# Kernel tuning notes

Measured on AMD Instinct MI355X. Metric: run time of the kernel, lower is better.

Reference implementation:

```python
import jax, jax.numpy as jnp
import numpy as np

NUM_POINTS = 100000
BATCH = 4096
K = 10


def setup_inputs() -> dict:
    key = jax.random.key(0)
    k1, k2, k3, k4, k5 = jax.random.split(key, 5)
    rays_o = jax.random.normal(k1, (BATCH, 3), dtype=jnp.float32)
    rays_d = jax.random.normal(k2, (BATCH, 3), dtype=jnp.float32)
    xyz = jax.random.normal(k3, (NUM_POINTS, 3), dtype=jnp.float32) * 0.1
    features_dc = jax.random.normal(k4, (NUM_POINTS, 1, 3), dtype=jnp.float32)
    opacity = jax.random.normal(k5, (NUM_POINTS, 1), dtype=jnp.float32)
    return {"rays_o": rays_o, "rays_d": rays_d, "xyz": xyz,
            "features_dc": features_dc, "opacity": opacity}


def reference(rays_o, rays_d, xyz, features_dc, opacity):
    # colors = sigmoid(features[:,0,:]) ; features[:,0,:] == features_dc[:,0,:]
    colors = jax.nn.sigmoid(features_dc[:, 0, :])          # [N,3]
    op = jax.nn.sigmoid(opacity[:, 0])                      # [N]
    ray_centers = rays_o + rays_d * 3.0                     # [B,3]
    # Euclidean cdist via ||a||^2 + ||b||^2 - 2 a.b (matmul form, like torch.cdist p=2)
    sq = (jnp.sum(ray_centers * ray_centers, axis=1)[:, None]
          + jnp.sum(xyz * xyz, axis=1)[None, :]
          - 2.0 * ray_centers @ xyz.T)                      # [B,N]
    distances = jnp.sqrt(jnp.maximum(sq, 0.0))
    # top-K smallest distances per ray
    _, idx = jax.lax.top_k(-distances, K)                   # [B,K]
    d_sel = jnp.take_along_axis(distances, idx, axis=1)     # [B,K]
    w = jnp.exp(-d_sel * 0.1) * op[idx]                     # [B,K]
    w = w / (jnp.sum(w, axis=1, keepdims=True) + 1e-8)
    rgb = jnp.einsum('bk,bkc->bc', w, colors[idx])          # [B,3]
    return rgb
```

## Files before the change

kernel.cpp:

```cpp
#include <hip/hip_runtime.h>
#include <math.h>

#define NPTS   100000
#define NRAYS  4096
#define KTOP   10
#define KMER   12
#define CAP    128
#define LCAP   12

#define PPAIR  4
#define SBLK   49
#define RCS    64
#define RPBS   (NRAYS / RCS)

#define TPAIR  4
#define NPART  64
#define TRAYS  8
#define TGRP   16

typedef float v2f __attribute__((ext_vector_type(2)));

static_assert(SBLK * 2048 >= NPTS, "scan covers all points");
static_assert(TGRP * 2048 <= NPTS, "theta sample within real points");

__device__ __forceinline__ float4 make_center(const float* __restrict__ ro,
                                              const float* __restrict__ rd,
                                              int ray, float w) {
    float ox = ro[3 * ray + 0], oy = ro[3 * ray + 1], oz = ro[3 * ray + 2];
    float dx = rd[3 * ray + 0], dy = rd[3 * ray + 1], dz = rd[3 * ray + 2];
    float cx, cy, cz;
    {
#pragma clang fp contract(off)
        cx = ox + dx * 3.0f;
        cy = oy + dy * 3.0f;
        cz = oz + dz * 3.0f;
    }
    return make_float4(cx, cy, cz, w);
}

__device__ __forceinline__ float sigm(float x) { return 1.0f / (1.0f + expf(-x)); }

__device__ __forceinline__ float rfl(float x) {
    return __int_as_float(__builtin_amdgcn_readfirstlane(__float_as_int(x)));
}

__device__ __forceinline__ v2f score2(v2f px, v2f py, v2f pz, v2f pw,
                                      v2f rx, v2f ry, v2f rz) {
    v2f t = __builtin_elementwise_fma(pz, rz, pw);
    t = __builtin_elementwise_fma(py, ry, t);
    return __builtin_elementwise_fma(px, rx, t);
}

__device__ __forceinline__ unsigned long long mkkey(float sc, int id, bool v) {
    unsigned u = __float_as_uint(sc);
    u = (u & 0x80000000u) ? ~u : (u | 0x80000000u);
    unsigned long long k = ((unsigned long long)u << 32) | (unsigned)(~id);
    return v ? k : 0ull;
}

__global__ __launch_bounds__(256, 2) void theta_kernel(const float* __restrict__ xyz,
                                                       const float* __restrict__ ro,
                                                       const float* __restrict__ rd,
                                                       float4* __restrict__ c4,
                                                       int* __restrict__ cnt) {
    __shared__ float4 rsh[TRAYS];
    __shared__ float  Msh[4][TRAYS][64];
    const int tid = threadIdx.x, wave = tid >> 6, lane = tid & 63;
    const int rbase = blockIdx.x * TRAYS;

    if (tid < TRAYS) rsh[tid] = make_center(ro, rd, rbase + tid, 0.0f);
    __syncthreads();

    float4 rr[TRAYS];
#pragma unroll
    for (int r = 0; r < TRAYS; ++r) rr[r] = rsh[r];

    v2f M[TRAYS];
#pragma unroll
    for (int r = 0; r < TRAYS; ++r) M[r] = (v2f){-INFINITY, -INFINITY};

#pragma unroll 1
    for (int g = 0; g < TGRP; g += 2) {
        v2f px[2][TPAIR], py[2][TPAIR], pz[2][TPAIR], pw[2][TPAIR];
#pragma unroll
        for (int h = 0; h < 2; ++h) {
            const int id0 = (g + h) * 2048 + wave * 512 + lane;
#pragma unroll
            for (int u = 0; u < TPAIR; ++u) {
                int ia = id0 + (2 * u) * 64, ib = id0 + (2 * u + 1) * 64;
                float xa = xyz[3 * ia + 0], ya = xyz[3 * ia + 1], za = xyz[3 * ia + 2];
                float xb = xyz[3 * ib + 0], yb = xyz[3 * ib + 1], zb = xyz[3 * ib + 2];
                px[h][u] = (v2f){xa, xb}; py[h][u] = (v2f){ya, yb}; pz[h][u] = (v2f){za, zb};
                pw[h][u] = (v2f){-0.5f * fmaf(xa, xa, fmaf(ya, ya, za * za)),
                                 -0.5f * fmaf(xb, xb, fmaf(yb, yb, zb * zb))};
            }
        }
#pragma unroll
        for (int r = 0; r < TRAYS; ++r) {
            const v2f rx = (v2f){rr[r].x, rr[r].x};
            const v2f ry = (v2f){rr[r].y, rr[r].y};
            const v2f rz = (v2f){rr[r].z, rr[r].z};
            v2f m = M[r];
#pragma unroll
            for (int h = 0; h < 2; ++h) {
#pragma unroll
                for (int u = 0; u < TPAIR; ++u) {
                    v2f t = __builtin_elementwise_fma(pz[h][u], rz, pw[h][u]);
                    t = __builtin_elementwise_fma(py[h][u], ry, t);
                    t = __builtin_elementwise_fma(px[h][u], rx, t);
                    m = __builtin_elementwise_max(m, t);
                }
            }
            M[r] = m;
        }
    }

#pragma unroll
    for (int r = 0; r < TRAYS; ++r)
        Msh[wave][r][lane] = fmaxf(M[r].x, M[r].y);
    __syncthreads();

    if (tid < TRAYS) {
        float vs[KTOP];
#pragma unroll
        for (int j = 0; j < KTOP; ++j) vs[j] = -INFINITY;
#pragma unroll 1
        for (int p = 0; p < NPART; ++p) {
            float v = fmaxf(fmaxf(Msh[0][tid][p], Msh[1][tid][p]),
                            fmaxf(Msh[2][tid][p], Msh[3][tid][p]));
#pragma unroll
            for (int t = KTOP - 1; t >= 1; --t) {
                bool up = v > vs[t - 1], here = v > vs[t];
                vs[t] = up ? vs[t - 1] : (here ? v : vs[t]);
            }
            vs[0] = fmaxf(vs[0], v);
        }
        float4 c = rsh[tid];
        c.w = vs[KTOP - 1];
        c4[rbase + tid] = c;
        cnt[rbase + tid] = 0;
    }
}

__global__ __launch_bounds__(256, 6) void scan_kernel(const float* __restrict__ xyz,
                                                      const float4* __restrict__ c4,
                                                      int* __restrict__ cnt,
                                                      float2* __restrict__ cand) {
    __shared__ int    lcnt[RPBS];
    __shared__ float2 lbuf[RPBS][LCAP];
    const int pblk = blockIdx.x, rchunk = blockIdx.y;
    const int tid = threadIdx.x, wave = tid >> 6, lane = tid & 63;
    const int rbase = rchunk * RPBS;

    if (tid < RPBS) lcnt[tid] = 0;

    const int id0 = pblk * 2048 + wave * 512 + lane;
    v2f px[PPAIR], py[PPAIR], pz[PPAIR], pw[PPAIR];
#pragma unroll
    for (int u = 0; u < PPAIR; ++u) {
        int ia = id0 + (2 * u) * 64, ib = id0 + (2 * u + 1) * 64;
        bool va = ia < NPTS, vb = ib < NPTS;
        int ca = va ? ia : 0, cb = vb ? ib : 0;
        float xa = xyz[3 * ca + 0], ya = xyz[3 * ca + 1], za = xyz[3 * ca + 2];
        float xb = xyz[3 * cb + 0], yb = xyz[3 * cb + 1], zb = xyz[3 * cb + 2];
        px[u] = (v2f){xa, xb}; py[u] = (v2f){ya, yb}; pz[u] = (v2f){za, zb};
        pw[u] = (v2f){va ? -0.5f * fmaf(xa, xa, fmaf(ya, ya, za * za)) : -INFINITY,
                      vb ? -0.5f * fmaf(xb, xb, fmaf(yb, yb, zb * zb)) : -INFINITY};
    }
    __syncthreads();

    auto emit = [&](int r, float sc, int id) {
        int slot = atomicAdd(&lcnt[r], 1);
        float2 e = make_float2(sc, __int_as_float(id));
        if (slot < LCAP) lbuf[r][slot] = e;
        else {
            int gs = atomicAdd(&cnt[rbase + r], 1);
            if (gs < CAP) cand[((rbase + r) << 7) + gs] = e;
        }
    };

#pragma unroll 1
    for (int rb = 0; rb < RPBS; rb += 4) {
        float4 q[4];
#pragma unroll
        for (int j = 0; j < 4; ++j) q[j] = c4[rbase + rb + j];
#pragma unroll
        for (int j = 0; j < 4; ++j) {
            const float cx = rfl(q[j].x), cy = rfl(q[j].y);
            const float cz = rfl(q[j].z), th = rfl(q[j].w);
            const v2f rx = (v2f){cx, cx}, ry = (v2f){cy, cy}, rz = (v2f){cz, cz};
            v2f t0 = score2(px[0], py[0], pz[0], pw[0], rx, ry, rz);
            v2f t1 = score2(px[1], py[1], pz[1], pw[1], rx, ry, rz);
            v2f t2 = score2(px[2], py[2], pz[2], pw[2], rx, ry, rz);
            v2f t3 = score2(px[3], py[3], pz[3], pw[3], rx, ry, rz);
            v2f am = __builtin_elementwise_max(__builtin_elementwise_max(t0, t1),
                                               __builtin_elementwise_max(t2, t3));
            float hm = fmaxf(am.x, am.y);

            if (__ballot(hm >= th)) {
                const int r = rb + j;
                if (t0.x >= th) emit(r, t0.x, id0 + 0 * 64);
                if (t0.y >= th) emit(r, t0.y, id0 + 1 * 64);
                if (t1.x >= th) emit(r, t1.x, id0 + 2 * 64);
                if (t1.y >= th) emit(r, t1.y, id0 + 3 * 64);
                if (t2.x >= th) emit(r, t2.x, id0 + 4 * 64);
                if (t2.y >= th) emit(r, t2.y, id0 + 5 * 64);
                if (t3.x >= th) emit(r, t3.x, id0 + 6 * 64);
                if (t3.y >= th) emit(r, t3.y, id0 + 7 * 64);
            }
        }
    }

    __syncthreads();
    if (tid < RPBS) {
        int n = lcnt[tid];
        n = n < LCAP ? n : LCAP;
        if (n > 0) {
            const int rayid = rbase + tid;
            int base = atomicAdd(&cnt[rayid], n);
            for (int j = 0; j < n; ++j) {
                int slot = base + j;
                if (slot < CAP) cand[(rayid << 7) + slot] = lbuf[tid][j];
            }
        }
    }
}

__global__ __launch_bounds__(256) void merge_kernel(const float* __restrict__ ro,
                                                    const float* __restrict__ rd,
                                                    const int* __restrict__ cnt,
                                                    const float2* __restrict__ cand,
                                                    const float* __restrict__ xyz,
                                                    const float* __restrict__ fdc,
                                                    const float* __restrict__ opac,
                                                    float* __restrict__ out) {
    const int wave = threadIdx.x >> 6, lane = threadIdx.x & 63;
    const int ray = blockIdx.x * 4 + wave;

    int n = cnt[ray];
    n = n < CAP ? n : CAP;

    const float2* cl = cand + (ray << 7);
    float2 e0 = cl[lane];
    float2 e1 = cl[64 + lane];
    int id0 = __float_as_int(e0.y), id1 = __float_as_int(e1.y);

    unsigned long long k0 = mkkey(e0.x, id0, lane < n);
    unsigned long long k1 = mkkey(e1.x, id1, lane + 64 < n);

    int sel = -1;
    unsigned long long kl = k0 > k1 ? k0 : k1;
#pragma unroll
    for (int j = 0; j < KMER; ++j) {
        unsigned long long m = kl;
#pragma unroll
        for (int off = 1; off < 64; off <<= 1) {
            unsigned long long o = __shfl_xor(m, off);
            m = m > o ? m : o;
        }
        bool win = (kl == m) && (m != 0ull);
        int wid = (k0 >= k1) ? id0 : id1;
        unsigned long long wmask = __ballot(win);
        int wl = __ffsll(wmask) - 1;
        int bid = __shfl(wid, wl & 63);
        if (m == 0ull) bid = -1;
        if (lane == j) sel = bid;
        if (win) {
            if (k0 >= k1) k0 = 0ull; else k1 = 0ull;
            kl = k0 > k1 ? k0 : k1;
        }
    }

    float ox = ro[3 * ray + 0], oy = ro[3 * ray + 1], oz = ro[3 * ray + 2];
    float dx = rd[3 * ray + 0], dy = rd[3 * ray + 1], dz = rd[3 * ray + 2];
    float cxf, cyf, czf;
    {
#pragma clang fp contract(off)
        cxf = ox + dx * 3.0f;
        cyf = oy + dy * 3.0f;
        czf = oz + dz * 3.0f;
    }
    double Cx = (double)cxf, Cy = (double)cyf, Cz = (double)czf;
    double cn = Cx * Cx + Cy * Cy + Cz * Cz;

    bool valid = (lane < KMER) && (sel >= 0);
    int pid = valid ? sel : 0;
    double X = (double)xyz[3 * pid + 0];
    double Y = (double)xyz[3 * pid + 1];
    double Z = (double)xyz[3 * pid + 2];
    double sq = valid ? (cn + (X * X + Y * Y + Z * Z) - 2.0 * (Cx * X + Cy * Y + Cz * Z))
                      : (double)INFINITY;
    int cid = valid ? sel : 0x7fffffff;

    int rank = 0;
#pragma unroll
    for (int k = 0; k < KMER; ++k) {
        double sk = __shfl(sq, k);
        int    ik = __shfl(cid, k);
        if ((sk < sq) || (sk == sq && ik < cid)) ++rank;
    }

    bool take = valid && (rank < KTOP);
    float w = 0.0f, rr = 0.0f, gg = 0.0f, bb = 0.0f;
    if (take) {
        float dd = sqrtf(fmaxf((float)sq, 0.0f));
        w  = expf(-0.1f * dd) * sigm(opac[pid]);
        rr = w * sigm(fdc[3 * pid + 0]);
        gg = w * sigm(fdc[3 * pid + 1]);
        bb = w * sigm(fdc[3 * pid + 2]);
    }
#pragma unroll
    for (int off = 1; off < 64; off <<= 1) {
        w  += __shfl_xor(w,  off);
        rr += __shfl_xor(rr, off);
        gg += __shfl_xor(gg, off);
        bb += __shfl_xor(bb, off);
    }
    if (lane == 0) {
        float inv = 1.0f / (w + 1e-8f);
        out[3 * ray + 0] = rr * inv;
        out[3 * ray + 1] = gg * inv;
        out[3 * ray + 2] = bb * inv;
    }
}

extern "C" void kernel_launch(void* const* d_in, const int* in_sizes, int n_in,
                              void* d_out, int out_size, void* d_ws, size_t ws_size,
                              hipStream_t stream) {
    const float* rays_o = (const float*)d_in[0];
    const float* rays_d = (const float*)d_in[1];
    const float* xyz    = (const float*)d_in[2];
    const float* fdc    = (const float*)d_in[3];
    const float* opac   = (const float*)d_in[4];
    float* out = (float*)d_out;

    char* w = (char*)d_ws;
    float4* c4   = (float4*)w;   w += (size_t)NRAYS * 16;
    int*    cnt  = (int*)w;      w += (size_t)NRAYS * 4;
    float2* cand = (float2*)w;

    theta_kernel<<<NRAYS / TRAYS, 256, 0, stream>>>(xyz, rays_o, rays_d, c4, cnt);
    scan_kernel<<<dim3(SBLK, RCS), 256, 0, stream>>>(xyz, c4, cnt, cand);
    merge_kernel<<<NRAYS / 4, 256, 0, stream>>>(rays_o, rays_d, cnt, cand, xyz, fdc, opac, out);
}
```

Measured before the change: 154.4 us.

## Double-buffer point loads in theta kernel and stage ray params in LDS for scan

The theta kernel now software-pipelines its point loads with two register buffers, so the next group's global loads are issued before the current group's FMAs run. The scan kernel copies the chunk's ray parameters into shared memory once and prefetches them four rays ahead instead of reading them from global memory every iteration. The scan kernel's max reduction is regrouped and its launch-bounds occupancy hint drops from 6 to 4 to leave room for the extra registers. The cost is higher register pressure and possibly lower occupancy.

Measured after the change: 152.7 us. About the same (-1.1%).

```diff
diff --git a/kernel.cpp b/kernel.cpp
--- a/kernel.cpp
+++ b/kernel.cpp
@@ -79,22 +79,22 @@
 #pragma unroll
     for (int r = 0; r < TRAYS; ++r) M[r] = (v2f){-INFINITY, -INFINITY};
 
-#pragma unroll 1
-    for (int g = 0; g < TGRP; g += 2) {
-        v2f px[2][TPAIR], py[2][TPAIR], pz[2][TPAIR], pw[2][TPAIR];
-#pragma unroll
-        for (int h = 0; h < 2; ++h) {
-            const int id0 = (g + h) * 2048 + wave * 512 + lane;
-#pragma unroll
-            for (int u = 0; u < TPAIR; ++u) {
-                int ia = id0 + (2 * u) * 64, ib = id0 + (2 * u + 1) * 64;
-                float xa = xyz[3 * ia + 0], ya = xyz[3 * ia + 1], za = xyz[3 * ia + 2];
-                float xb = xyz[3 * ib + 0], yb = xyz[3 * ib + 1], zb = xyz[3 * ib + 2];
-                px[h][u] = (v2f){xa, xb}; py[h][u] = (v2f){ya, yb}; pz[h][u] = (v2f){za, zb};
-                pw[h][u] = (v2f){-0.5f * fmaf(xa, xa, fmaf(ya, ya, za * za)),
-                                 -0.5f * fmaf(xb, xb, fmaf(yb, yb, zb * zb))};
-            }
-        }
+    v2f pxA[TPAIR], pyA[TPAIR], pzA[TPAIR], pwA[TPAIR];
+    v2f pxB[TPAIR], pyB[TPAIR], pzB[TPAIR], pwB[TPAIR];
+
+    auto loadg = [&](v2f* PX, v2f* PY, v2f* PZ, v2f* PW, int g) {
+        const int id0 = g * 2048 + wave * 512 + lane;
+#pragma unroll
+        for (int u = 0; u < TPAIR; ++u) {
+            int ia = id0 + (2 * u) * 64, ib = id0 + (2 * u + 1) * 64;
+            float xa = xyz[3 * ia + 0], ya = xyz[3 * ia + 1], za = xyz[3 * ia + 2];
+            float xb = xyz[3 * ib + 0], yb = xyz[3 * ib + 1], zb = xyz[3 * ib + 2];
+            PX[u] = (v2f){xa, xb}; PY[u] = (v2f){ya, yb}; PZ[u] = (v2f){za, zb};
+            PW[u] = (v2f){-0.5f * fmaf(xa, xa, fmaf(ya, ya, za * za)),
+                          -0.5f * fmaf(xb, xb, fmaf(yb, yb, zb * zb))};
+        }
+    };
+    auto computeg = [&](const v2f* PX, const v2f* PY, const v2f* PZ, const v2f* PW) {
 #pragma unroll
         for (int r = 0; r < TRAYS; ++r) {
             const v2f rx = (v2f){rr[r].x, rr[r].x};
@@ -102,17 +102,19 @@
             const v2f rz = (v2f){rr[r].z, rr[r].z};
             v2f m = M[r];
 #pragma unroll
-            for (int h = 0; h < 2; ++h) {
-#pragma unroll
-                for (int u = 0; u < TPAIR; ++u) {
-                    v2f t = __builtin_elementwise_fma(pz[h][u], rz, pw[h][u]);
-                    t = __builtin_elementwise_fma(py[h][u], ry, t);
-                    t = __builtin_elementwise_fma(px[h][u], rx, t);
-                    m = __builtin_elementwise_max(m, t);
-                }
-            }
+            for (int u = 0; u < TPAIR; ++u)
+                m = __builtin_elementwise_max(m, score2(PX[u], PY[u], PZ[u], PW[u], rx, ry, rz));
             M[r] = m;
         }
+    };
+
+    loadg(pxA, pyA, pzA, pwA, 0);
+#pragma unroll 1
+    for (int g = 0; g < TGRP; g += 2) {
+        loadg(pxB, pyB, pzB, pwB, g + 1);
+        computeg(pxA, pyA, pzA, pwA);
+        if (g + 2 < TGRP) loadg(pxA, pyA, pzA, pwA, g + 2);
+        computeg(pxB, pyB, pzB, pwB);
     }
 
 #pragma unroll
@@ -142,17 +144,21 @@
     }
 }
 
-__global__ __launch_bounds__(256, 6) void scan_kernel(const float* __restrict__ xyz,
+__global__ __launch_bounds__(256, 4) void scan_kernel(const float* __restrict__ xyz,
                                                       const float4* __restrict__ c4,
                                                       int* __restrict__ cnt,
                                                       float2* __restrict__ cand) {
+    __shared__ float4 lsh[RPBS];
     __shared__ int    lcnt[RPBS];
     __shared__ float2 lbuf[RPBS][LCAP];
     const int pblk = blockIdx.x, rchunk = blockIdx.y;
     const int tid = threadIdx.x, wave = tid >> 6, lane = tid & 63;
     const int rbase = rchunk * RPBS;
 
-    if (tid < RPBS) lcnt[tid] = 0;
+    if (tid < RPBS) {
+        lsh[tid] = c4[rbase + tid];
+        lcnt[tid] = 0;
+    }
 
     const int id0 = pblk * 2048 + wave * 512 + lane;
     v2f px[PPAIR], py[PPAIR], pz[PPAIR], pw[PPAIR];
@@ -179,36 +185,44 @@
         }
     };
 
+    auto do_ray = [&](int r, float4 rp) {
+        const float cx = rfl(rp.x), cy = rfl(rp.y);
+        const float cz = rfl(rp.z), th = rfl(rp.w);
+        const v2f rx = (v2f){cx, cx}, ry = (v2f){cy, cy}, rz = (v2f){cz, cz};
+        v2f t0 = score2(px[0], py[0], pz[0], pw[0], rx, ry, rz);
+        v2f t1 = score2(px[1], py[1], pz[1], pw[1], rx, ry, rz);
+        v2f t2 = score2(px[2], py[2], pz[2], pw[2], rx, ry, rz);
+        v2f t3 = score2(px[3], py[3], pz[3], pw[3], rx, ry, rz);
+        float m1 = fmaxf(fmaxf(t0.x, t0.y), t1.x);
+        float m2 = fmaxf(fmaxf(t1.y, t2.x), t2.y);
+        float m3 = fmaxf(fmaxf(t3.x, t3.y), m1);
+        float hm = fmaxf(m3, m2);
+
+        if (__ballot(hm >= th)) {
+            if (t0.x >= th) emit(r, t0.x, id0 + 0 * 64);
+            if (t0.y >= th) emit(r, t0.y, id0 + 1 * 64);
+            if (t1.x >= th) emit(r, t1.x, id0 + 2 * 64);
+            if (t1.y >= th) emit(r, t1.y, id0 + 3 * 64);
+            if (t2.x >= th) emit(r, t2.x, id0 + 4 * 64);
+            if (t2.y >= th) emit(r, t2.y, id0 + 5 * 64);
+            if (t3.x >= th) emit(r, t3.x, id0 + 6 * 64);
+            if (t3.y >= th) emit(r, t3.y, id0 + 7 * 64);
+        }
+    };
+
+    float4 A0 = lsh[0], A1 = lsh[1], A2 = lsh[2], A3 = lsh[3];
 #pragma unroll 1
-    for (int rb = 0; rb < RPBS; rb += 4) {
-        float4 q[4];
-#pragma unroll
-        for (int j = 0; j < 4; ++j) q[j] = c4[rbase + rb + j];
-#pragma unroll
-        for (int j = 0; j < 4; ++j) {
-            const float cx = rfl(q[j].x), cy = rfl(q[j].y);
-            const float cz = rfl(q[j].z), th = rfl(q[j].w);
-            const v2f rx = (v2f){cx, cx}, ry = (v2f){cy, cy}, rz = (v2f){cz, cz};
-            v2f t0 = score2(px[0], py[0], pz[0], pw[0], rx, ry, rz);
-            v2f t1 = score2(px[1], py[1], pz[1], pw[1], rx, ry, rz);
-            v2f t2 = score2(px[2], py[2], pz[2], pw[2], rx, ry, rz);
-            v2f t3 = score2(px[3], py[3], pz[3], pw[3], rx, ry, rz);
-            v2f am = __builtin_elementwise_max(__builtin_elementwise_max(t0, t1),
-                                               __builtin_elementwise_max(t2, t3));
-            float hm = fmaxf(am.x, am.y);
-
-            if (__ballot(hm >= th)) {
-                const int r = rb + j;
-                if (t0.x >= th) emit(r, t0.x, id0 + 0 * 64);
-                if (t0.y >= th) emit(r, t0.y, id0 + 1 * 64);
-                if (t1.x >= th) emit(r, t1.x, id0 + 2 * 64);
-                if (t1.y >= th) emit(r, t1.y, id0 + 3 * 64);
-                if (t2.x >= th) emit(r, t2.x, id0 + 4 * 64);
-                if (t2.y >= th) emit(r, t2.y, id0 + 5 * 64);
-                if (t3.x >= th) emit(r, t3.x, id0 + 6 * 64);
-                if (t3.y >= th) emit(r, t3.y, id0 + 7 * 64);
-            }
-        }
+    for (int rb = 0; rb < RPBS; rb += 8) {
+        float4 B0 = lsh[rb + 4], B1 = lsh[rb + 5];
+        float4 B2 = lsh[rb + 6], B3 = lsh[rb + 7];
+        do_ray(rb + 0, A0); do_ray(rb + 1, A1);
+        do_ray(rb + 2, A2); do_ray(rb + 3, A3);
+        if (rb + 8 < RPBS) {
+            A0 = lsh[rb + 8];  A1 = lsh[rb + 9];
+            A2 = lsh[rb + 10]; A3 = lsh[rb + 11];
+        }
+        do_ray(rb + 4, B0); do_ray(rb + 5, B1);
+        do_ray(rb + 6, B2); do_ray(rb + 7, B3);
     }
 
     __syncthreads();
```
